# Kernel tuning notes

Hardware: AMD Instinct MI355X
Metric: run time of the kernel (lower is better)

## Reference

```python
import jax, jax.numpy as jnp
import numpy as np

BLOCK = 64
THRESH = 0.95
EPS = 1e-8


def setup_inputs() -> dict:
    key = jax.random.key(0)
    kq, kk, kv = jax.random.split(key, 3)
    S, D = 4096, 128
    q = jax.random.normal(kq, (S, D), dtype=jnp.float32)
    k = jax.random.normal(kk, (S, D), dtype=jnp.float32)
    v = jax.random.normal(kv, (S, D), dtype=jnp.float32)
    return {"q": q, "k": k, "v": v}


def reference(q, k, v):
    S, D = q.shape
    nb = S // BLOCK
    qb = q.reshape(nb, BLOCK, D)
    kb = k.reshape(nb, BLOCK, D)
    vb = v.reshape(nb, BLOCK, D)
    # all block-pair scores: [nb_q, nb_k, BLOCK_q, BLOCK_k]
    scores = jnp.einsum('ibd,jcd->ijbc', qb, kb)
    m = jnp.max(scores, axis=-1, keepdims=True)
    e = jnp.exp(scores - m)
    s = jnp.sum(e, axis=-1, keepdims=True)  # per-block-pair softmax denominator
    # top-p truncation mask: sort descending, cumsum, threshold
    srt = jnp.sort(e, axis=-1)[..., ::-1]
    cum = jnp.cumsum(srt, axis=-1)
    mask = cum < THRESH * s
    # NOTE: faithful to original — mask (in sorted order) is applied to the
    # UNSORTED exp_scores, exactly as the torch code does (indices unused).
    em = e * mask
    em = em / (jnp.sum(em, axis=-1, keepdims=True) + EPS)
    # accumulate over key blocks j (per-pair normalized weights, summed)
    out = jnp.einsum('ijbc,jcd->ibd', em, vb)
    return out.reshape(S, D)
```

## Files before the change

kernel.cpp:

```cpp
#include <hip/hip_runtime.h>
#include <cstdint>
#include <cstddef>


#define SEQ   4096
#define DIM   128
#define BLK   64
#define NB    (SEQ / BLK)
#define NJG   16
#define JPB   (NB / NJG)
#define NT    256
#define PSTR  12288
#define THRESH 0.95f
#define EPSF   1e-8f

typedef __attribute__((ext_vector_type(8))) _Float16 f16x8;
typedef __attribute__((ext_vector_type(4))) float    f32x4;

#define MFMAH(a, b, c) __builtin_amdgcn_mfma_f32_16x16x32_f16((a), (b), (c), 0, 0, 0)

union UH4 { uint2 u; _Float16 h[4]; };
union UH8 { uint4 u; f16x8 v; };

__device__ __forceinline__ void gll16(const uint* g, uint* l) {
  __builtin_amdgcn_global_load_lds(
      (const __attribute__((address_space(1))) void*)g,
      (__attribute__((address_space(3))) void*)l, 16, 0, 0);
}

__global__ __launch_bounds__(NT, 4) void eco_prep_kernel(
    const float* __restrict__ K, const float* __restrict__ V,
    uint* __restrict__ P, float* __restrict__ O) {
  const int tid  = threadIdx.x;
  const int b    = blockIdx.x;
  const int jb   = b >> 2;
  const int part = b & 3;

  {
    float4 z = {0.f, 0.f, 0.f, 0.f};
    float4* op = (float4*)O;
#pragma unroll
    for (int it = 0; it < 2; ++it) op[b * 512 + it * NT + tid] = z;
  }

  {
    const float4* gk = (const float4*)(K + (size_t)jb * BLK * DIM);
    uint* dst = P + (size_t)jb * PSTR;
#pragma unroll
    for (int it = 0; it < 2; ++it) {
      int f = part * 512 + it * NT + tid;
      int r = f >> 5, c4 = f & 31;
      float4 x = gk[f];
      float xs[4] = {x.x, x.y, x.z, x.w};
      UH4 uh, ur;
#pragma unroll
      for (int e = 0; e < 4; ++e) {
        float v = xs[e];
        _Float16 h = (_Float16)v;
        uh.h[e] = h;
        ur.h[e] = (_Float16)(v - (float)h);
      }
      uint off = (uint)r * 64u + (((uint)(c4 >> 1) ^ (uint)(r & 15)) << 2) +
                 (uint)((c4 & 1) << 1);
      *(uint2*)&dst[off]        = uh.u;
      *(uint2*)&dst[4096 + off] = ur.u;
    }
  }

  {
    const float* gv = V + (size_t)jb * BLK * DIM;
    uint4* dv = (uint4*)(P + (size_t)jb * PSTR + 8192);
    int idx = part * 256 + tid;
    int ch = idx >> 7, d = idx & 127;
    UH8 u;
#pragma unroll
    for (int j = 0; j < 8; ++j)
      u.v[j] = (_Float16)gv[(ch * 8 + j) * DIM + d];
    dv[idx] = u.u;
  }
}

#define CE(x, y, dmax) { float _hi = fmaxf((x), (y)); float _lo = fminf((x), (y)); \
                         (x) = (dmax) ? _hi : _lo; (y) = (dmax) ? _lo : _hi; }

__global__ __launch_bounds__(NT, 4) void eco_attn_kernel(
    const float* __restrict__ Q, const uint* __restrict__ P,
    float* __restrict__ O) {
  __shared__ __align__(16) uint sK[8192];
  __shared__ __align__(16) uint sW[2048];

  const int tid  = threadIdx.x;
  const int ib   = blockIdx.y;
  const int jg   = blockIdx.x;
  const int lane = tid & 63;
  const int wv   = tid >> 6;
  const int quad = lane >> 4;
  const int l16  = lane & 15;
  const int q4   = quad << 2;

  uint* sWw = sW + wv * 512;

  f16x8 qh[4], qr[4];
  {
    const float* qp = Q + (size_t)(ib * BLK + wv * 16 + l16) * DIM + quad * 8;
#pragma unroll
    for (int ks = 0; ks < 4; ++ks) {
      float4 x0 = *(const float4*)(qp + ks * 32);
      float4 x1 = *(const float4*)(qp + ks * 32 + 4);
      float xs[8] = {x0.x, x0.y, x0.z, x0.w, x1.x, x1.y, x1.z, x1.w};
      f16x8 h8, r8;
#pragma unroll
      for (int e = 0; e < 8; ++e) {
        float v = xs[e];
        _Float16 h = (_Float16)v;
        h8[e] = h;
        r8[e] = (_Float16)(v - (float)h);
      }
      qh[ks] = h8; qr[ks] = r8;
    }
  }

  const f32x4 zf = {0.f, 0.f, 0.f, 0.f};
  f32x4 pv[8];
#pragma unroll
  for (int i = 0; i < 8; ++i) pv[i] = zf;

  {
    const uint* gsrc = P + (size_t)(jg * JPB) * PSTR;
#pragma unroll
    for (int it = 0; it < 8; ++it) {
      int idx = (it * NT + tid) << 2;
      gll16(gsrc + idx, sK + idx);
    }
  }

  for (int jj = 0; jj < JPB; ++jj) {
    const int jb = jg * JPB + jj;
    __syncthreads();

    f32x4 ah[4], ar[4];
#pragma unroll
    for (int nt = 0; nt < 4; ++nt) { ah[nt] = zf; ar[nt] = zf; }
#pragma unroll
    for (int nt = 0; nt < 4; ++nt) {
      const int rB = nt * 16 + l16;
      const uint rowoff = (uint)rB * 64u;
      const uint swk = (uint)(rB & 15);
#pragma unroll
      for (int ks = 0; ks < 4; ++ks) {
        uint off = rowoff + ((((uint)(ks * 4 + quad)) ^ swk) << 2);
        f16x8 bh = *(const f16x8*)&sK[off];
        f16x8 br = *(const f16x8*)&sK[4096 + off];
        ah[nt] = MFMAH(bh, qh[ks], ah[nt]);
        ar[nt] = MFMAH(br, qh[ks], ar[nt]);
        ar[nt] = MFMAH(bh, qr[ks], ar[nt]);
      }
    }
    __syncthreads();

    if (jj + 1 < JPB) {
      const uint* gsrc = P + (size_t)(jb + 1) * PSTR;
#pragma unroll
      for (int it = 0; it < 8; ++it) {
        int idx = (it * NT + tid) << 2;
        gll16(gsrc + idx, sK + idx);
      }
    }

    {
      float a[16], e[16];
#pragma unroll
      for (int nt = 0; nt < 4; ++nt) {
        f32x4 s = ah[nt] + ar[nt];
#pragma unroll
        for (int rg = 0; rg < 4; ++rg) a[nt * 4 + rg] = s[rg];
      }
      float mt[8];
#pragma unroll
      for (int i = 0; i < 8; ++i) mt[i] = fmaxf(a[i], a[i + 8]);
#pragma unroll
      for (int w2 = 4; w2 >= 1; w2 >>= 1)
#pragma unroll
        for (int i = 0; i < w2; ++i) mt[i] = fmaxf(mt[i], mt[i + w2]);
      float m = mt[0];
      m = fmaxf(m, __shfl_xor(m, 16, 64));
      m = fmaxf(m, __shfl_xor(m, 32, 64));
#pragma unroll
      for (int i = 0; i < 16; ++i) { a[i] = __expf(a[i] - m); e[i] = a[i]; }
      float st[8];
#pragma unroll
      for (int i = 0; i < 8; ++i) st[i] = a[i] + a[i + 8];
#pragma unroll
      for (int w2 = 4; w2 >= 1; w2 >>= 1)
#pragma unroll
        for (int i = 0; i < w2; ++i) st[i] += st[i + w2];
      float sr = st[0];
      sr += __shfl_xor(sr, 16, 64);
      sr += __shfl_xor(sr, 32, 64);
      const float T = THRESH * sr;

      const int s = quad;
#pragma unroll
      for (int k2 = 2; k2 <= 8; k2 <<= 1)
#pragma unroll
        for (int j2 = k2 >> 1; j2 >= 1; j2 >>= 1)
#pragma unroll
          for (int i = 0; i < 16; ++i) {
            int l = i ^ j2;
            if (l > i) { bool d = ((i & k2) == 0); CE(a[i], a[l], d); }
          }
      const bool x16 = ((s & 1) == 0);
      const bool x32 = ((s & 2) == 0);
#pragma unroll
      for (int j2 = 8; j2 >= 1; j2 >>= 1)
#pragma unroll
        for (int i = 0; i < 16; ++i) {
          int l = i ^ j2;
          if (l > i) { CE(a[i], a[l], x16); }
        }
      {
        const bool km = (x32 == x16);
#pragma unroll
        for (int i = 0; i < 16; ++i) {
          float o = __shfl_xor(a[i], 16, 64);
          a[i] = km ? fmaxf(a[i], o) : fminf(a[i], o);
        }
#pragma unroll
        for (int j2 = 8; j2 >= 1; j2 >>= 1)
#pragma unroll
          for (int i = 0; i < 16; ++i) {
            int l = i ^ j2;
            if (l > i) { CE(a[i], a[l], x32); }
          }
      }
      {
#pragma unroll
        for (int i = 0; i < 16; ++i) {
          float o = __shfl_xor(a[i], 32, 64);
          a[i] = x32 ? fmaxf(a[i], o) : fminf(a[i], o);
        }
#pragma unroll
        for (int i = 0; i < 16; ++i) {
          float o = __shfl_xor(a[i], 16, 64);
          a[i] = x16 ? fmaxf(a[i], o) : fminf(a[i], o);
        }
#pragma unroll
        for (int j2 = 8; j2 >= 1; j2 >>= 1)
#pragma unroll
          for (int i = 0; i < 16; ++i) {
            int l = i ^ j2;
            if (l > i) { CE(a[i], a[l], true); }
          }
      }
#pragma unroll
      for (int i = 1; i < 16; ++i) a[i] += a[i - 1];
      float tot = a[15];
      float c = tot;
      float o1 = __shfl_up(c, 16, 64); if (s >= 1) c += o1;
      float o2 = __shfl_up(c, 32, 64); if (s >= 2) c += o2;
      const float excl = c - tot;
      int cnt = 0;
#pragma unroll
      for (int i = 0; i < 16; ++i) cnt += ((a[i] + excl) < T) ? 1 : 0;
      cnt += __shfl_xor(cnt, 16, 64);
      cnt += __shfl_xor(cnt, 32, 64);
      const int t = cnt;
      float p = 0.f;
#pragma unroll
      for (int i = 0; i < 16; ++i) {
        int kidx = ((i >> 2) << 4) + q4 + (i & 3);
        p += (kidx < t) ? e[i] : 0.f;
      }
      p += __shfl_xor(p, 16, 64);
      p += __shfl_xor(p, 32, 64);
      const float rn = 1.0f / (p + EPSF);
      uint* wrow = sWw + l16 * 32;
#pragma unroll
      for (int nt = 0; nt < 4; ++nt) {
        UH4 u;
#pragma unroll
        for (int rg = 0; rg < 4; ++rg) {
          int kidx = nt * 16 + q4 + rg;
          float w = (kidx < t) ? e[nt * 4 + rg] * rn : 0.f;
          u.h[rg] = (_Float16)w;
        }
        uint c4 = (uint)(nt * 4 + quad);
        *(uint2*)&wrow[(c4 ^ (uint)l16) << 1] = u.u;
      }
    }
    __builtin_amdgcn_wave_barrier();

    f16x8 wf[2];
#pragma unroll
    for (int ks2 = 0; ks2 < 2; ++ks2) {
      uint c0 = (uint)(ks2 * 8 + quad * 2);
      const uint* wrow = sWw + l16 * 32;
      uint2 lo = *(const uint2*)&wrow[(c0 ^ (uint)l16) << 1];
      uint2 hi = *(const uint2*)&wrow[((c0 + 1) ^ (uint)l16) << 1];
      UH8 u;
      u.u = make_uint4(lo.x, lo.y, hi.x, hi.y);
      wf[ks2] = u.v;
    }
    {
      const uint* gvt = P + (size_t)jb * PSTR + 8192;
#pragma unroll
      for (int nt2 = 0; nt2 < 8; ++nt2) {
#pragma unroll
        for (int ks2 = 0; ks2 < 2; ++ks2) {
          f16x8 vf = *(const f16x8*)&gvt[((uint)((ks2 * 4 + quad) * 128 +
                                                 nt2 * 16 + l16)) << 2];
          pv[nt2] = MFMAH(wf[ks2], vf, pv[nt2]);
        }
      }
    }
  }

#pragma unroll
  for (int nt2 = 0; nt2 < 8; ++nt2) {
    const int col  = nt2 * 16 + l16;
    const int row0 = ib * BLK + wv * 16 + quad * 4;
#pragma unroll
    for (int rg = 0; rg < 4; ++rg)
      atomicAdd(O + (size_t)(row0 + rg) * DIM + col, pv[nt2][rg]);
  }
}

extern "C" void kernel_launch(void* const* d_in, const int* in_sizes, int n_in,
                              void* d_out, int out_size, void* d_ws, size_t ws_size,
                              hipStream_t stream) {
  (void)in_sizes; (void)n_in; (void)ws_size; (void)out_size;
  const float* q = (const float*)d_in[0];
  const float* k = (const float*)d_in[1];
  const float* v = (const float*)d_in[2];
  float* out = (float*)d_out;
  uint* prep = (uint*)d_ws;

  eco_prep_kernel<<<dim3(NB * 4), dim3(NT), 0, stream>>>(k, v, prep, out);
  eco_attn_kernel<<<dim3(NJG, NB), dim3(NT), 0, stream>>>(q, prep, out);
}
```

Measured before the change: 118.6 us.

## Replace bitonic sort with iterative max extraction for top-p cutoff

Instead of fully sorting each 64-element row of exponentiated scores with a bitonic network and prefix-summing, the kernel repeatedly extracts the wave-wide maximum and accumulates it until the cumulative mass crosses the threshold. It starts from the known row maximum of 1 and loops only while any row is still below threshold. This aims to cut the large compare-exchange and shuffle cost when few elements are needed, at the price of a data-dependent loop and slightly different handling of tied values.

```diff
diff --git a/kernel.cpp b/kernel.cpp
--- a/kernel.cpp
+++ b/kernel.cpp
@@ -80,9 +80,6 @@
   }
 }
 
-#define CE(x, y, dmax) { float _hi = fmaxf((x), (y)); float _lo = fminf((x), (y)); \
-                         (x) = (dmax) ? _hi : _lo; (y) = (dmax) ? _lo : _hi; }
-
 __global__ __launch_bounds__(NT, 4) void eco_attn_kernel(
     const float* __restrict__ Q, const uint* __restrict__ P,
     float* __restrict__ O) {
@@ -199,72 +196,31 @@
       sr += __shfl_xor(sr, 32, 64);
       const float T = THRESH * sr;
 
-      const int s = quad;
-#pragma unroll
-      for (int k2 = 2; k2 <= 8; k2 <<= 1)
-#pragma unroll
-        for (int j2 = k2 >> 1; j2 >= 1; j2 >>= 1)
-#pragma unroll
-          for (int i = 0; i < 16; ++i) {
-            int l = i ^ j2;
-            if (l > i) { bool d = ((i & k2) == 0); CE(a[i], a[l], d); }
-          }
-      const bool x16 = ((s & 1) == 0);
-      const bool x32 = ((s & 2) == 0);
-#pragma unroll
-      for (int j2 = 8; j2 >= 1; j2 >>= 1)
-#pragma unroll
-        for (int i = 0; i < 16; ++i) {
-          int l = i ^ j2;
-          if (l > i) { CE(a[i], a[l], x16); }
+      float cum = 1.0f;
+      bool live = (cum < T);
+      int t = live ? 1 : 0;
+#pragma unroll
+      for (int i = 0; i < 16; ++i) a[i] = (a[i] >= 1.0f) ? 0.f : a[i];
+      while (__any(live)) {
+        float M = fmaxf(fmaxf(fmaxf(a[0], a[1]), a[2]),
+                        fmaxf(fmaxf(a[3], a[4]), a[5]));
+        M = fmaxf(M, fmaxf(fmaxf(a[6],  a[7]),  a[8]));
+        M = fmaxf(M, fmaxf(fmaxf(a[9],  a[10]), a[11]));
+        M = fmaxf(M, fmaxf(fmaxf(a[12], a[13]), a[14]));
+        M = fmaxf(M, a[15]);
+        M = fmaxf(M, __shfl_xor(M, 16, 64));
+        M = fmaxf(M, __shfl_xor(M, 32, 64));
+        const float cn = cum + M;
+        const bool cross = !(cn < T) || !(M > 0.f);
+        if (live) {
+          cum = cn;
+          t += cross ? 0 : 1;
         }
-      {
-        const bool km = (x32 == x16);
-#pragma unroll
-        for (int i = 0; i < 16; ++i) {
-          float o = __shfl_xor(a[i], 16, 64);
-          a[i] = km ? fmaxf(a[i], o) : fminf(a[i], o);
-        }
-#pragma unroll
-        for (int j2 = 8; j2 >= 1; j2 >>= 1)
-#pragma unroll
-          for (int i = 0; i < 16; ++i) {
-            int l = i ^ j2;
-            if (l > i) { CE(a[i], a[l], x32); }
-          }
-      }
-      {
-#pragma unroll
-        for (int i = 0; i < 16; ++i) {
-          float o = __shfl_xor(a[i], 32, 64);
-          a[i] = x32 ? fmaxf(a[i], o) : fminf(a[i], o);
-        }
-#pragma unroll
-        for (int i = 0; i < 16; ++i) {
-          float o = __shfl_xor(a[i], 16, 64);
-          a[i] = x16 ? fmaxf(a[i], o) : fminf(a[i], o);
-        }
-#pragma unroll
-        for (int j2 = 8; j2 >= 1; j2 >>= 1)
-#pragma unroll
-          for (int i = 0; i < 16; ++i) {
-            int l = i ^ j2;
-            if (l > i) { CE(a[i], a[l], true); }
-          }
-      }
-#pragma unroll
-      for (int i = 1; i < 16; ++i) a[i] += a[i - 1];
-      float tot = a[15];
-      float c = tot;
-      float o1 = __shfl_up(c, 16, 64); if (s >= 1) c += o1;
-      float o2 = __shfl_up(c, 32, 64); if (s >= 2) c += o2;
-      const float excl = c - tot;
-      int cnt = 0;
-#pragma unroll
-      for (int i = 0; i < 16; ++i) cnt += ((a[i] + excl) < T) ? 1 : 0;
-      cnt += __shfl_xor(cnt, 16, 64);
-      cnt += __shfl_xor(cnt, 32, 64);
-      const int t = cnt;
+        live = live && !cross;
+#pragma unroll
+        for (int i = 0; i < 16; ++i) a[i] = (a[i] >= M) ? 0.f : a[i];
+      }
+
       float p = 0.f;
 #pragma unroll
       for (int i = 0; i < 16; ++i) {
```

Result: slower. 125.1 us (+5.5%).

## Replace full bitonic sort with iterative top-max extraction and skip upper PV half

Applied to the files above, without the earlier changes.

Before falling back to the full cross-lane bitonic sort, each row peels off its largest exp values (the max is exactly 1) in four max-extraction passes and accumulates the cumulative sum. The sort runs only if some row in the wave has not yet crossed the threshold. The kept-key count is also reduced across the wave, and when no row keeps more than 32 keys the upper half of the weight writes and the second set of PV MFMAs and V loads are skipped. This trades a data-dependent branch and extra max passes for avoiding sort and MFMA work when the distribution is peaked. Ties at equal values may count differently from the sorted cumsum.

```diff
diff --git a/kernel.cpp b/kernel.cpp
--- a/kernel.cpp
+++ b/kernel.cpp
@@ -167,13 +167,15 @@
       }
     }
 
+    bool doHi;
+
     {
       float a[16], e[16];
 #pragma unroll
       for (int nt = 0; nt < 4; ++nt) {
-        f32x4 s = ah[nt] + ar[nt];
-#pragma unroll
-        for (int rg = 0; rg < 4; ++rg) a[nt * 4 + rg] = s[rg];
+        f32x4 sc = ah[nt] + ar[nt];
+#pragma unroll
+        for (int rg = 0; rg < 4; ++rg) a[nt * 4 + rg] = sc[rg];
       }
       float mt[8];
 #pragma unroll
@@ -199,72 +201,108 @@
       sr += __shfl_xor(sr, 32, 64);
       const float T = THRESH * sr;
 
-      const int s = quad;
-#pragma unroll
-      for (int k2 = 2; k2 <= 8; k2 <<= 1)
-#pragma unroll
-        for (int j2 = k2 >> 1; j2 >= 1; j2 >>= 1)
+      float cum = 1.0f;
+      bool live = (cum < T);
+      int t = live ? 1 : 0;
+#pragma unroll
+      for (int i = 0; i < 16; ++i) a[i] = (a[i] >= 1.0f) ? 0.f : a[i];
+#pragma unroll
+      for (int p4 = 0; p4 < 4; ++p4) {
+        float M = fmaxf(fmaxf(fmaxf(a[0], a[1]), a[2]),
+                        fmaxf(fmaxf(a[3], a[4]), a[5]));
+        M = fmaxf(M, fmaxf(fmaxf(a[6],  a[7]),  a[8]));
+        M = fmaxf(M, fmaxf(fmaxf(a[9],  a[10]), a[11]));
+        M = fmaxf(M, fmaxf(fmaxf(a[12], a[13]), a[14]));
+        M = fmaxf(M, a[15]);
+        M = fmaxf(M, __shfl_xor(M, 16, 64));
+        M = fmaxf(M, __shfl_xor(M, 32, 64));
+        const float cn = cum + M;
+        const bool cross = !(cn < T) || !(M > 0.f);
+        if (live) { cum = cn; t += cross ? 0 : 1; }
+        live = live && !cross;
+#pragma unroll
+        for (int i = 0; i < 16; ++i) a[i] = (a[i] >= M) ? 0.f : a[i];
+      }
+
+      if (__any(live)) {
+        const int s = quad;
+#pragma unroll
+        for (int k2 = 2; k2 <= 8; k2 <<= 1)
+#pragma unroll
+          for (int j2 = k2 >> 1; j2 >= 1; j2 >>= 1)
+#pragma unroll
+            for (int i = 0; i < 16; ++i) {
+              int l = i ^ j2;
+              if (l > i) { bool d = ((i & k2) == 0); CE(a[i], a[l], d); }
+            }
+        const bool x16 = ((s & 1) == 0);
+        const bool x32 = ((s & 2) == 0);
+#pragma unroll
+        for (int j2 = 8; j2 >= 1; j2 >>= 1)
 #pragma unroll
           for (int i = 0; i < 16; ++i) {
             int l = i ^ j2;
-            if (l > i) { bool d = ((i & k2) == 0); CE(a[i], a[l], d); }
+            if (l > i) { CE(a[i], a[l], x16); }
           }
-      const bool x16 = ((s & 1) == 0);
-      const bool x32 = ((s & 2) == 0);
-#pragma unroll
-      for (int j2 = 8; j2 >= 1; j2 >>= 1)
-#pragma unroll
-        for (int i = 0; i < 16; ++i) {
-          int l = i ^ j2;
-          if (l > i) { CE(a[i], a[l], x16); }
+        {
+          const bool km = (x32 == x16);
+#pragma unroll
+          for (int i = 0; i < 16; ++i) {
+            float o = __shfl_xor(a[i], 16, 64);
+            a[i] = km ? fmaxf(a[i], o) : fminf(a[i], o);
+          }
+#pragma unroll
+          for (int j2 = 8; j2 >= 1; j2 >>= 1)
+#pragma unroll
+            for (int i = 0; i < 16; ++i) {
+              int l = i ^ j2;
+              if (l > i) { CE(a[i], a[l], x32); }
+            }
         }
+        {
+#pragma unroll
+          for (int i = 0; i < 16; ++i) {
+            float o = __shfl_xor(a[i], 32, 64);
+            a[i] = x32 ? fmaxf(a[i], o) : fminf(a[i], o);
+          }
+#pragma unroll
+          for (int i = 0; i < 16; ++i) {
+            float o = __shfl_xor(a[i], 16, 64);
+            a[i] = x16 ? fmaxf(a[i], o) : fminf(a[i], o);
+          }
+#pragma unroll
+          for (int j2 = 8; j2 >= 1; j2 >>= 1)
+#pragma unroll
+            for (int i = 0; i < 16; ++i) {
+              int l = i ^ j2;
+              if (l > i) { CE(a[i], a[l], true); }
+            }
+        }
+#pragma unroll
+        for (int i = 1; i < 16; ++i) a[i] += a[i - 1];
+        float tot = a[15];
+        float c = tot;
+        float o1 = __shfl_up(c, 16, 64); if (s >= 1) c += o1;
+        float o2 = __shfl_up(c, 32, 64); if (s >= 2) c += o2;
+        const float excl = c - tot;
+        int cnt = 0;
+#pragma unroll
+        for (int i = 0; i < 16; ++i) cnt += ((cum + a[i] + excl) < T) ? 1 : 0;
+        cnt += __shfl_xor(cnt, 16, 64);
+        cnt += __shfl_xor(cnt, 32, 64);
+        if (live) t += cnt;
+      }
+
       {
-        const bool km = (x32 == x16);
-#pragma unroll
-        for (int i = 0; i < 16; ++i) {
-          float o = __shfl_xor(a[i], 16, 64);
-          a[i] = km ? fmaxf(a[i], o) : fminf(a[i], o);
-        }
-#pragma unroll
-        for (int j2 = 8; j2 >= 1; j2 >>= 1)
-#pragma unroll
-          for (int i = 0; i < 16; ++i) {
-            int l = i ^ j2;
-            if (l > i) { CE(a[i], a[l], x32); }
-          }
-      }
-      {
-#pragma unroll
-        for (int i = 0; i < 16; ++i) {
-          float o = __shfl_xor(a[i], 32, 64);
-          a[i] = x32 ? fmaxf(a[i], o) : fminf(a[i], o);
-        }
-#pragma unroll
-        for (int i = 0; i < 16; ++i) {
-          float o = __shfl_xor(a[i], 16, 64);
-          a[i] = x16 ? fmaxf(a[i], o) : fminf(a[i], o);
-        }
-#pragma unroll
-        for (int j2 = 8; j2 >= 1; j2 >>= 1)
-#pragma unroll
-          for (int i = 0; i < 16; ++i) {
-            int l = i ^ j2;
-            if (l > i) { CE(a[i], a[l], true); }
-          }
-      }
-#pragma unroll
-      for (int i = 1; i < 16; ++i) a[i] += a[i - 1];
-      float tot = a[15];
-      float c = tot;
-      float o1 = __shfl_up(c, 16, 64); if (s >= 1) c += o1;
-      float o2 = __shfl_up(c, 32, 64); if (s >= 2) c += o2;
-      const float excl = c - tot;
-      int cnt = 0;
-#pragma unroll
-      for (int i = 0; i < 16; ++i) cnt += ((a[i] + excl) < T) ? 1 : 0;
-      cnt += __shfl_xor(cnt, 16, 64);
-      cnt += __shfl_xor(cnt, 32, 64);
-      const int t = cnt;
+        int tm = t;
+        int o;
+        o = __shfl_xor(tm, 1, 64); tm = (o > tm) ? o : tm;
+        o = __shfl_xor(tm, 2, 64); tm = (o > tm) ? o : tm;
+        o = __shfl_xor(tm, 4, 64); tm = (o > tm) ? o : tm;
+        o = __shfl_xor(tm, 8, 64); tm = (o > tm) ? o : tm;
+        doHi = (tm > 32);
+      }
+
       float p = 0.f;
 #pragma unroll
       for (int i = 0; i < 16; ++i) {
@@ -276,7 +314,7 @@
       const float rn = 1.0f / (p + EPSF);
       uint* wrow = sWw + l16 * 32;
 #pragma unroll
-      for (int nt = 0; nt < 4; ++nt) {
+      for (int nt = 0; nt < 2; ++nt) {
         UH4 u;
 #pragma unroll
         for (int rg = 0; rg < 4; ++rg) {
@@ -287,30 +325,52 @@
         uint c4 = (uint)(nt * 4 + quad);
         *(uint2*)&wrow[(c4 ^ (uint)l16) << 1] = u.u;
       }
+      if (doHi) {
+#pragma unroll
+        for (int nt = 2; nt < 4; ++nt) {
+          UH4 u;
+#pragma unroll
+          for (int rg = 0; rg < 4; ++rg) {
+            int kidx = nt * 16 + q4 + rg;
+            float w = (kidx < t) ? e[nt * 4 + rg] * rn : 0.f;
+            u.h[rg] = (_Float16)w;
+          }
+          uint c4 = (uint)(nt * 4 + quad);
+          *(uint2*)&wrow[(c4 ^ (uint)l16) << 1] = u.u;
+        }
+      }
     }
     __builtin_amdgcn_wave_barrier();
 
-    f16x8 wf[2];
-#pragma unroll
-    for (int ks2 = 0; ks2 < 2; ++ks2) {
-      uint c0 = (uint)(ks2 * 8 + quad * 2);
+    const uint* gvt = P + (size_t)jb * PSTR + 8192;
+    {
+      uint c0 = (uint)(quad * 2);
       const uint* wrow = sWw + l16 * 32;
       uint2 lo = *(const uint2*)&wrow[(c0 ^ (uint)l16) << 1];
       uint2 hi = *(const uint2*)&wrow[((c0 + 1) ^ (uint)l16) << 1];
       UH8 u;
       u.u = make_uint4(lo.x, lo.y, hi.x, hi.y);
-      wf[ks2] = u.v;
-    }
-    {
-      const uint* gvt = P + (size_t)jb * PSTR + 8192;
+      f16x8 wf0 = u.v;
 #pragma unroll
       for (int nt2 = 0; nt2 < 8; ++nt2) {
-#pragma unroll
-        for (int ks2 = 0; ks2 < 2; ++ks2) {
-          f16x8 vf = *(const f16x8*)&gvt[((uint)((ks2 * 4 + quad) * 128 +
-                                                 nt2 * 16 + l16)) << 2];
-          pv[nt2] = MFMAH(wf[ks2], vf, pv[nt2]);
-        }
+        f16x8 vf = *(const f16x8*)&gvt[((uint)(quad * 128 +
+                                               nt2 * 16 + l16)) << 2];
+        pv[nt2] = MFMAH(wf0, vf, pv[nt2]);
+      }
+    }
+    if (doHi) {
+      uint c0 = (uint)(8 + quad * 2);
+      const uint* wrow = sWw + l16 * 32;
+      uint2 lo = *(const uint2*)&wrow[(c0 ^ (uint)l16) << 1];
+      uint2 hi = *(const uint2*)&wrow[((c0 + 1) ^ (uint)l16) << 1];
+      UH8 u;
+      u.u = make_uint4(lo.x, lo.y, hi.x, hi.y);
+      f16x8 wf1 = u.v;
+#pragma unroll
+      for (int nt2 = 0; nt2 < 8; ++nt2) {
+        f16x8 vf = *(const f16x8*)&gvt[((uint)((4 + quad) * 128 +
+                                               nt2 * 16 + l16)) << 2];
+        pv[nt2] = MFMAH(wf1, vf, pv[nt2]);
       }
     }
   }
```

Result: no change. 116.4 us (-1.9%).
